# Kernel optimization log

Measured on AMD Instinct MI355X. Metric: run time of the kernel, lower is better.

Reference implementation:

```python
import jax, jax.numpy as jnp
import numpy as np

B, D, L, K = 4096, 1280, 16384, 64


def setup_inputs() -> dict:
    key = jax.random.key(0)
    k1, k2, k3, k4, k5 = jax.random.split(key, 5)
    scale_enc = 1.0 / np.sqrt(D)
    scale_dec = 1.0 / np.sqrt(L)
    return {
        "x_BD": jax.random.normal(k1, (B, D), dtype=jnp.float32),
        "pb_D": jax.random.normal(k2, (D,), dtype=jnp.float32) * 0.01,
        "W_enc": jax.random.normal(k3, (D, L), dtype=jnp.float32) * scale_enc,
        "lb_L": jax.random.normal(k4, (L,), dtype=jnp.float32) * 0.01,
        "W_dec": jax.random.normal(k5, (L, D), dtype=jnp.float32) * scale_dec,
    }


def topk_activation(x_BL, k):
    # lax.top_k over last dim, relu the values, scatter back into zeros
    tv_Bk, ti_Bk = jax.lax.top_k(x_BL, k)
    tv_Bk = jax.nn.relu(tv_Bk)
    b_B = jnp.arange(x_BL.shape[0])[:, None]
    return jnp.zeros_like(x_BL).at[b_B, ti_Bk].set(tv_Bk)


def reference(x_BD, pb_D, W_enc, lb_L, W_dec):
    # encode: shift by pre-bias, dense, add latent bias
    xshift_BD = x_BD - pb_D
    zpre_BL = xshift_BD @ W_enc + lb_L          # [B, L]
    # top-k sparse activation
    z_BL = topk_activation(zpre_BL, K)          # [B, L], only K nonzeros per row
    # decode: dense matmul over full L (the kernel-headroom target)
    xhat_BD = z_BL @ W_dec + pb_D               # [B, D]
    return (zpre_BL, z_BL, xhat_BD)
```

## Files before the change

### kernel.cpp

```cpp
#include <hip/hip_runtime.h>
#include <hip/hip_bf16.h>
#include <stdint.h>

#define B_SZ 4096
#define D_SZ 1280
#define L_SZ 16384
#define K_TOP 64
#define C_CAP 192
#define BAND 0.07f
#define CL_CAP 512
#define T_COLLECT 2.2f

typedef __attribute__((ext_vector_type(8))) short s16x8;
typedef __attribute__((ext_vector_type(4))) float f32x4;

#define GLOAD_LDS16(gp, lp)                                                          \
  __builtin_amdgcn_global_load_lds((const __attribute__((address_space(1))) void*)(gp), \
                                   (__attribute__((address_space(3))) void*)(lp), 16, 0, 0)

static __device__ __forceinline__ unsigned short f2bf(float f) {
  __hip_bfloat16 h = __float2bfloat16(f);
  return *reinterpret_cast<unsigned short*>(&h);
}
static __device__ __forceinline__ float bf2f(unsigned short u) {
  return __uint_as_float((unsigned)u << 16);
}
static __device__ __forceinline__ unsigned mkkey(float f) {
  const unsigned u = __float_as_uint(f);
  return (u & 0x80000000u) ? ~u : (u | 0x80000000u);
}
static __device__ __forceinline__ float unkey(unsigned k) {
  const unsigned u = (k & 0x80000000u) ? (k & 0x7fffffffu) : ~k;
  return __uint_as_float(u);
}
static __device__ __forceinline__ void nt_store4(const float4& v, float4* p) {
  f32x4 x;
  x[0] = v.x; x[1] = v.y; x[2] = v.z; x[3] = v.w;
  __builtin_nontemporal_store(x, (f32x4*)p);
}

__global__ __launch_bounds__(256) void sae_prep(const float* __restrict__ x,
                                                const float* __restrict__ pb,
                                                const float* __restrict__ We,
                                                const float* __restrict__ Wd,
                                                unsigned short* __restrict__ A,
                                                float* __restrict__ xs,
                                                float* __restrict__ WT,
                                                unsigned short* __restrict__ WbT,
                                                unsigned short* __restrict__ Wdb,
                                                int* __restrict__ bk_cnt,
                                                int* __restrict__ cl_cnt) {
  const int b = blockIdx.x, t = threadIdx.x;
  if (b < 5120) {
    __shared__ float tile[64][65];
    const int l0 = (b & 255) * 64, d0 = (b >> 8) * 64;
    const int c = t & 63, rg = t >> 6;
#pragma unroll
    for (int i = 0; i < 16; ++i) {
      const int row = i * 4 + rg;
      tile[row][c] = We[(size_t)(d0 + row) * L_SZ + l0 + c];
    }
    __syncthreads();
#pragma unroll
    for (int i = 0; i < 16; ++i) {
      const int row = i * 4 + rg;
      const float v = tile[c][row];
      const size_t o = (size_t)(l0 + row) * D_SZ + d0 + c;
      WT[o] = v;
      WbT[o] = f2bf(v);
    }
  } else if (b < 5120 + 4096) {
    const int r = b - 5120;
    const float* xr = x + (size_t)r * D_SZ;
    unsigned short* ar = A + (size_t)r * D_SZ;
    float* sr = xs + (size_t)r * D_SZ;
    for (int d = t; d < D_SZ; d += 256) {
      const float v = xr[d] - pb[d];
      ar[d] = f2bf(v);
      sr[d] = v;
    }
  } else if (b < 5120 + 4096 + 2048) {
    const int n4 = L_SZ * D_SZ / 4;
    for (int i = (b - 9216) * 256 + t; i < n4; i += 2048 * 256) {
      const float4 v = ((const float4*)Wd)[i];
      ushort4 o;
      o.x = f2bf(v.x); o.y = f2bf(v.y); o.z = f2bf(v.z); o.w = f2bf(v.w);
      ((ushort4*)Wdb)[i] = o;
    }
  } else if (b < 11328) {
    bk_cnt[(b - 11264) * 256 + t] = 0;
  } else {
    cl_cnt[(b - 11328) * 256 + t] = 0;
  }
}

#define SWZ(lin) ((lin) ^ ((((lin) >> 7) & 7) << 4))
#define A_LDS 0
#define B_LDS 65536
#define KBYTES (D_SZ * 2)

#define PH_MID()                                          \
  __builtin_amdgcn_s_barrier();                           \
  asm volatile("s_waitcnt lgkmcnt(0)" ::: "memory");      \
  __builtin_amdgcn_sched_barrier(0);                      \
  __builtin_amdgcn_s_setprio(1)

#define PH_END()                                          \
  __builtin_amdgcn_s_setprio(0);                          \
  __builtin_amdgcn_s_barrier();                           \
  __builtin_amdgcn_sched_barrier(0)

__global__ __launch_bounds__(512, 1) void sae_gemm(const unsigned short* __restrict__ A,
                                                   const unsigned short* __restrict__ WT,
                                                   const float* __restrict__ lb,
                                                   float* __restrict__ zpre,
                                                   int* __restrict__ cl_cnt,
                                                   int* __restrict__ cl_idx,
                                                   float* __restrict__ cl_val) {
  __shared__ short lds[65536];
  char* ldsc = (char*)lds;
  const int t = threadIdx.x, lane = t & 63, w = t >> 6;
  const int wr = w >> 2, wc = w & 3, w2 = w * 2;

  const int bid = blockIdx.x;
  const int xcd = bid & 7, i2 = bid >> 3;
  const int b2 = i2 >> 4, inner = i2 & 15;
  const int mt = (b2 & 3) * 4 + (inner & 3);
  const int nt = xcd * 8 + (b2 >> 2) * 4 + (inner >> 2);
  const int m0 = mt * 256, n0 = nt * 256;

  f32x4 acc[8][4] = {};

  auto STAGE = [&](const unsigned short* op, int rowbase, int ldsop, int buf, int half, int tile) {
#pragma unroll
    for (int s = 0; s < 2; ++s) {
      const int o = (w2 + s) * 1024 + lane * 16;
      const int r = o >> 7;
      const int cb = (o & 127) ^ (((o >> 7) & 7) << 4);
      const char* g = (const char*)op + (size_t)(rowbase + half * 128 + r) * KBYTES +
                      tile * 128 + cb;
      char* l = ldsc + ldsop + buf * 32768 + half * 16384 + (w2 + s) * 1024;
      GLOAD_LDS16(g, l);
    }
  };
  auto LDA = [&](s16x8* af, int buf, int q) {
#pragma unroll
    for (int i = 0; i < 2; ++i)
#pragma unroll
      for (int kk = 0; kk < 2; ++kk) {
        const int r = (q * 2 + i) * 16 + (lane & 15);
        int lin = r * 128 + kk * 64 + ((lane >> 4) * 16);
        lin = SWZ(lin);
        af[i * 2 + kk] = *(const s16x8*)(ldsc + A_LDS + buf * 32768 + wr * 16384 + lin);
      }
  };
  auto LDB = [&](s16x8* bg, int buf) {
#pragma unroll
    for (int j = 0; j < 4; ++j)
#pragma unroll
      for (int kk = 0; kk < 2; ++kk) {
        const int nloc = wc * 64 + j * 16 + (lane & 15);
        const int half = nloc >> 7, r = nloc & 127;
        int lin = r * 128 + kk * 64 + ((lane >> 4) * 16);
        lin = SWZ(lin);
        bg[j * 2 + kk] = *(const s16x8*)(ldsc + B_LDS + buf * 32768 + half * 16384 + lin);
      }
  };
  auto MM = [&](s16x8* af, s16x8* bg, int q) {
#pragma unroll
    for (int i = 0; i < 2; ++i)
#pragma unroll
      for (int j = 0; j < 4; ++j)
#pragma unroll
        for (int kk = 0; kk < 2; ++kk)
          acc[q * 2 + i][j] =
              __builtin_amdgcn_mfma_f32_16x16x32_bf16(af[i * 2 + kk], bg[j * 2 + kk],
                                                      acc[q * 2 + i][j], 0, 0, 0);
  };

  STAGE(WT, n0, B_LDS, 0, 0, 0); STAGE(WT, n0, B_LDS, 0, 1, 0);
  STAGE(A, m0, A_LDS, 0, 0, 0);  STAGE(A, m0, A_LDS, 0, 1, 0);
  STAGE(WT, n0, B_LDS, 1, 0, 1); STAGE(WT, n0, B_LDS, 1, 1, 1);
  asm volatile("s_waitcnt vmcnt(4)" ::: "memory");
  __builtin_amdgcn_s_barrier();
  __builtin_amdgcn_sched_barrier(0);

  const int NI = D_SZ / 128;
  for (int i = 0; i < NI; ++i) {
    const bool last = (i == NI - 1);
    s16x8 af[4], bg[8];
    LDB(bg, 0); LDA(af, 0, 0);
    STAGE(A, m0, A_LDS, 1, 0, 2 * i + 1); STAGE(A, m0, A_LDS, 1, 1, 2 * i + 1);
    PH_MID(); MM(af, bg, 0); PH_END();
    LDA(af, 0, 1);
    if (!last) STAGE(WT, n0, B_LDS, 0, 0, 2 * i + 2);
    PH_MID(); MM(af, bg, 1); PH_END();
    LDA(af, 0, 2);
    if (!last) STAGE(WT, n0, B_LDS, 0, 1, 2 * i + 2);
    PH_MID(); MM(af, bg, 2); PH_END();
    LDA(af, 0, 3);
    PH_MID(); MM(af, bg, 3);
    __builtin_amdgcn_s_setprio(0);
    if (last) { asm volatile("s_waitcnt vmcnt(0)" ::: "memory"); }
    else      { asm volatile("s_waitcnt vmcnt(4)" ::: "memory"); }
    __builtin_amdgcn_s_barrier();
    __builtin_amdgcn_sched_barrier(0);
    LDB(bg, 1); LDA(af, 1, 0);
    if (!last) STAGE(A, m0, A_LDS, 0, 0, 2 * i + 2);
    PH_MID(); MM(af, bg, 0); PH_END();
    LDA(af, 1, 1);
    if (!last) STAGE(A, m0, A_LDS, 0, 1, 2 * i + 2);
    PH_MID(); MM(af, bg, 1); PH_END();
    LDA(af, 1, 2);
    if (!last) STAGE(WT, n0, B_LDS, 1, 0, 2 * i + 3);
    PH_MID(); MM(af, bg, 2); PH_END();
    LDA(af, 1, 3);
    if (!last) STAGE(WT, n0, B_LDS, 1, 1, 2 * i + 3);
    PH_MID(); MM(af, bg, 3);
    __builtin_amdgcn_s_setprio(0);
    asm volatile("s_waitcnt vmcnt(4)" ::: "memory");
    __builtin_amdgcn_s_barrier();
    __builtin_amdgcn_sched_barrier(0);
  }

  const int cl = lane & 15, rg = lane >> 4;
#pragma unroll
  for (int j = 0; j < 4; ++j) {
    const int cc = n0 + wc * 64 + j * 16 + cl;
    const float bias = lb[cc];
#pragma unroll
    for (int i = 0; i < 8; ++i) {
      const int row0 = m0 + wr * 128 + i * 16 + rg * 4;
      const size_t base = (size_t)row0 * L_SZ + cc;
#pragma unroll
      for (int tt = 0; tt < 4; ++tt) {
        const float v = acc[i][j][tt] + bias;
        __builtin_nontemporal_store(v, &zpre[base + (size_t)tt * L_SZ]);
        if (v >= T_COLLECT) {
          const int p = atomicAdd(&cl_cnt[row0 + tt], 1);
          if (p < CL_CAP) {
            cl_idx[(size_t)(row0 + tt) * CL_CAP + p] = cc;
            cl_val[(size_t)(row0 + tt) * CL_CAP + p] = v;
          }
        }
      }
    }
  }
}

__device__ void radix_pick(unsigned* hist, unsigned* suf, int* sh_b, unsigned* sh_above,
                           int target, int t) {
  if (t == 0) *sh_b = -1;
  unsigned p = hist[4 * t] + hist[4 * t + 1] + hist[4 * t + 2] + hist[4 * t + 3];
  suf[t] = p;
  for (int off = 1; off < 256; off <<= 1) {
    __syncthreads();
    unsigned v = (t + off < 256) ? suf[t + off] : 0u;
    __syncthreads();
    suf[t] += v;
  }
  __syncthreads();
  const unsigned shi = (t + 1 < 256) ? suf[t + 1] : 0u;
  unsigned S = shi;
  int best = -1;
#pragma unroll
  for (int i = 3; i >= 0; --i) {
    S += hist[4 * t + i];
    if (S >= (unsigned)target) { best = 4 * t + i; break; }
  }
  if (best >= 0) atomicMax(sh_b, best);
  __syncthreads();
  const int b = *sh_b;
  if ((b >> 2) == t) {
    unsigned above = shi;
    for (int i = 3; i > (b & 3); --i) above += hist[4 * t + i];
    *sh_above = above;
  }
  __syncthreads();
}

__device__ void radix_pick4(unsigned* hist4, unsigned* suf, int* sh_b, unsigned* sh_above,
                            int target, int t) {
  if (t == 0) *sh_b = -1;
  if (t < 256) {
    unsigned p = 0;
#pragma unroll
    for (int i = 0; i < 4; ++i)
#pragma unroll
      for (int c = 0; c < 4; ++c) p += hist4[(4 * t + i) * 4 + c];
    suf[t] = p;
  }
  for (int off = 1; off < 256; off <<= 1) {
    __syncthreads();
    unsigned v = (t < 256 && t + off < 256) ? suf[t + off] : 0u;
    __syncthreads();
    if (t < 256) suf[t] += v;
  }
  __syncthreads();
  if (t < 256) {
    const unsigned shi = (t + 1 < 256) ? suf[t + 1] : 0u;
    unsigned S = shi;
    int best = -1;
    for (int i = 3; i >= 0; --i) {
      unsigned cnt = 0;
#pragma unroll
      for (int c = 0; c < 4; ++c) cnt += hist4[(4 * t + i) * 4 + c];
      S += cnt;
      if (S >= (unsigned)target) { best = 4 * t + i; break; }
    }
    if (best >= 0) atomicMax(sh_b, best);
  }
  __syncthreads();
  const int b = *sh_b;
  if (t < 256 && (b >> 2) == t) {
    unsigned above = (t + 1 < 256) ? suf[t + 1] : 0u;
    for (int i = 3; i > (b & 3); --i) {
      unsigned cnt = 0;
#pragma unroll
      for (int c = 0; c < 4; ++c) cnt += hist4[(4 * t + i) * 4 + c];
      above += cnt;
    }
    *sh_above = above;
  }
  __syncthreads();
}

__global__ __launch_bounds__(512) void sae_mega(const float* __restrict__ zpre,
                                                const float* __restrict__ xs,
                                                const float* __restrict__ WT,
                                                const float* __restrict__ lb,
                                                const unsigned short* __restrict__ Wdb,
                                                const float* __restrict__ pb,
                                                const int* __restrict__ cl_cnt,
                                                const int* __restrict__ cl_idx,
                                                const float* __restrict__ cl_val,
                                                float* __restrict__ z,
                                                float* __restrict__ xhat) {
  __shared__ unsigned hist4[4096];
  __shared__ unsigned suf[256];
  __shared__ int l_idx[CL_CAP];
  __shared__ unsigned l_key[CL_CAP];
  __shared__ int sh_b0, sh_b1, sh_nhi, sh_nband;
  __shared__ unsigned sh_above, sh_v64k;
  __shared__ int bl[C_CAP];
  __shared__ float bfv[C_CAP];
  __shared__ double be[C_CAP];
  __shared__ int ids[K_TOP];
  __shared__ float vs[K_TOP];

  const int r = blockIdx.x, t = threadIdx.x, lane = t & 63, w = t >> 6;
  const float4* zr4 = (const float4*)(zpre + (size_t)r * L_SZ);

  float4 xc[5];
  {
    const float4* xr4 = (const float4*)(xs + (size_t)r * D_SZ);
#pragma unroll
    for (int i = 0; i < 5; ++i) xc[i] = xr4[lane + 64 * i];
  }

  if (t == 0) { sh_nhi = 0; sh_nband = 0; }
  const int n_raw = cl_cnt[r];
  bool fast = (n_raw >= K_TOP && n_raw <= CL_CAP);
  float lo_f = 0.f, hi_f = 0.f;

  if (fast) {
    for (int i = t; i < n_raw; i += 512) {
      l_idx[i] = cl_idx[(size_t)r * CL_CAP + i];
      l_key[i] = mkkey(cl_val[(size_t)r * CL_CAP + i]);
    }
    __syncthreads();
    if (t < n_raw) {
      const unsigned myk = l_key[t];
      const int myi = l_idx[t];
      int rank = 0;
      for (int j = 0; j < n_raw; ++j) {
        const unsigned kj = l_key[j];
        rank += (kj > myk || (kj == myk && l_idx[j] < myi)) ? 1 : 0;
      }
      if (rank == K_TOP - 1) sh_v64k = myk;
    }
    __syncthreads();
    const float v64f = unkey(sh_v64k);
    lo_f = v64f - BAND;
    hi_f = v64f + BAND;
    if (T_COLLECT > lo_f) fast = false;
  }
  __syncthreads();
  if (!fast) {
    for (int i = t; i < 4096; i += 512) hist4[i] = 0;
    __syncthreads();
    for (int i = t; i < L_SZ / 4; i += 512) {
      const float4 v = zr4[i];
      const float va[4] = {v.x, v.y, v.z, v.w};
#pragma unroll
      for (int q = 0; q < 4; ++q)
        atomicAdd(&hist4[(mkkey(va[q]) >> 22) * 4 + (lane & 3)], 1u);
    }
    __syncthreads();
    radix_pick4(hist4, suf, &sh_b0, &sh_above, K_TOP, t);
    const int b0 = sh_b0;
    const int tgt2 = K_TOP - (int)sh_above;
    for (int i = t; i < 4096; i += 512) hist4[i] = 0;
    __syncthreads();
    for (int i = t; i < L_SZ / 4; i += 512) {
      const float4 v = zr4[i];
      const float va[4] = {v.x, v.y, v.z, v.w};
#pragma unroll
      for (int q = 0; q < 4; ++q) {
        const unsigned k = mkkey(va[q]);
        if ((int)(k >> 22) == b0) atomicAdd(&hist4[((k >> 12) & 1023u) * 4 + (lane & 3)], 1u);
      }
    }
    __syncthreads();
    radix_pick4(hist4, suf, &sh_b1, &sh_above, tgt2, t);
    const unsigned v64lb_key = (((unsigned)b0 << 10) | (unsigned)sh_b1) << 12;
    lo_f = unkey(v64lb_key) - BAND;
    hi_f = unkey(v64lb_key + 4095u) + BAND;
  }
  __syncthreads();
  if (fast) {
    if (t < n_raw) {
      const float val = unkey(l_key[t]);
      if (val >= lo_f) {
        if (val > hi_f) {
          const int p = atomicAdd(&sh_nhi, 1);
          if (p < K_TOP) { ids[p] = l_idx[t]; vs[p] = fmaxf(val, 0.f); }
        } else {
          const int p = atomicAdd(&sh_nband, 1);
          if (p < C_CAP) { bl[p] = l_idx[t]; bfv[p] = val; }
        }
      }
    }
  } else {
    for (int i = t; i < L_SZ / 4; i += 512) {
      const float4 v = zr4[i];
      const float va[4] = {v.x, v.y, v.z, v.w};
#pragma unroll
      for (int q = 0; q < 4; ++q) {
        const float val = va[q];
        if (val >= lo_f) {
          if (val > hi_f) {
            const int p = atomicAdd(&sh_nhi, 1);
            if (p < K_TOP) { ids[p] = 4 * i + q; vs[p] = fmaxf(val, 0.f); }
          } else {
            const int p = atomicAdd(&sh_nband, 1);
            if (p < C_CAP) { bl[p] = 4 * i + q; bfv[p] = val; }
          }
        }
      }
    }
  }
  __syncthreads();
  const int nh = sh_nhi < K_TOP ? sh_nhi : K_TOP;
  const int nb = sh_nband < C_CAP ? sh_nband : C_CAP;
  for (int e = w; e < nb; e += 8) {
    const int l = bl[e];
    const float4* wr4 = (const float4*)(WT + (size_t)l * D_SZ);
    double acc = 0.0;
#pragma unroll
    for (int i = 0; i < 5; ++i) {
      const float4 wv = wr4[lane + 64 * i];
      acc += (double)xc[i].x * (double)wv.x + (double)xc[i].y * (double)wv.y +
             (double)xc[i].z * (double)wv.z + (double)xc[i].w * (double)wv.w;
    }
#pragma unroll
    for (int off = 32; off > 0; off >>= 1) acc += __shfl_down(acc, off);
    if (lane == 0) be[e] = acc + (double)lb[l];
  }
  __syncthreads();
  const int need = K_TOP - nh;
  if (t < nb) {
    const double ev = be[t];
    const int l = bl[t];
    int rank = 0;
    for (int j = 0; j < nb; ++j) {
      const double e2 = be[j];
      if (e2 > ev || (e2 == ev && bl[j] < l)) ++rank;
    }
    if (rank < need) {
      ids[nh + rank] = l;
      vs[nh + rank] = fmaxf(bfv[t], 0.f);
    }
  }
  __syncthreads();
  if (t < 320) {
    float4 acc = ((const float4*)pb)[t];
#pragma unroll 8
    for (int k = 0; k < K_TOP; ++k) {
      const ushort4 wv = ((const ushort4*)(Wdb + (size_t)ids[k] * D_SZ))[t];
      const float vk = vs[k];
      acc.x += vk * bf2f(wv.x);
      acc.y += vk * bf2f(wv.y);
      acc.z += vk * bf2f(wv.z);
      acc.w += vk * bf2f(wv.w);
    }
    nt_store4(acc, &((float4*)(xhat + (size_t)r * D_SZ))[t]);
  } else {
    const int tz = t - 320;
    float4* zr = (float4*)(z + (size_t)r * L_SZ);
    const float4 zero = make_float4(0.f, 0.f, 0.f, 0.f);
    for (int i = tz; i < L_SZ / 4; i += 192) nt_store4(zero, &zr[i]);
  }
  __syncthreads();
  if (t < K_TOP) __builtin_nontemporal_store(vs[t], &z[(size_t)r * L_SZ + ids[t]]);
}

__global__ __launch_bounds__(256) void sae_topc(const float* __restrict__ zpre,
                                                int* __restrict__ bk_cnt,
                                                int* __restrict__ band_lat,
                                                float* __restrict__ band_fval,
                                                int* __restrict__ n_hi,
                                                int* __restrict__ n_band,
                                                int* __restrict__ t_idx,
                                                float* __restrict__ t_val) {
  __shared__ unsigned hist[1024];
  __shared__ unsigned suf[256];
  __shared__ int sh_b0, sh_b1, sh_nhi, sh_nband;
  __shared__ unsigned sh_above;
  const int r = blockIdx.x, t = threadIdx.x;
  const float4* zr4 = (const float4*)(zpre + (size_t)r * L_SZ);

  for (int i = t; i < 1024; i += 256) hist[i] = 0;
  if (t == 0) { sh_nhi = 0; sh_nband = 0; }
  __syncthreads();
  for (int i = t; i < L_SZ / 4; i += 256) {
    const float4 v = zr4[i];
    atomicAdd(&hist[mkkey(v.x) >> 22], 1u);
    atomicAdd(&hist[mkkey(v.y) >> 22], 1u);
    atomicAdd(&hist[mkkey(v.z) >> 22], 1u);
    atomicAdd(&hist[mkkey(v.w) >> 22], 1u);
  }
  __syncthreads();
  radix_pick(hist, suf, &sh_b0, &sh_above, K_TOP, t);
  const int b0 = sh_b0;
  const int target2 = K_TOP - (int)sh_above;
  __syncthreads();
  for (int i = t; i < 1024; i += 256) hist[i] = 0;
  __syncthreads();
  for (int i = t; i < L_SZ / 4; i += 256) {
    const float4 v = zr4[i];
    const float va[4] = {v.x, v.y, v.z, v.w};
#pragma unroll
    for (int q = 0; q < 4; ++q) {
      const unsigned k = mkkey(va[q]);
      if ((int)(k >> 22) == b0) atomicAdd(&hist[(k >> 12) & 1023u], 1u);
    }
  }
  __syncthreads();
  radix_pick(hist, suf, &sh_b1, &sh_above, target2, t);
  const unsigned v64lb_key = (((unsigned)b0 << 10) | (unsigned)sh_b1) << 12;
  const float lo_f = unkey(v64lb_key) - BAND;
  const float hi_f = unkey(v64lb_key + 4095u) + BAND;
  __syncthreads();
  for (int i = t; i < L_SZ / 4; i += 256) {
    const float4 v = zr4[i];
    const float va[4] = {v.x, v.y, v.z, v.w};
#pragma unroll
    for (int q = 0; q < 4; ++q) {
      const float val = va[q];
      if (val >= lo_f) {
        const int l = 4 * i + q;
        if (val > hi_f) {
          const int p = atomicAdd(&sh_nhi, 1);
          if (p < K_TOP) {
            t_idx[(size_t)r * K_TOP + p] = l;
            t_val[(size_t)r * K_TOP + p] = fmaxf(val, 0.f);
          }
        } else {
          const int p = atomicAdd(&sh_nband, 1);
          if (p < C_CAP) {
            band_lat[(r << 8) + p] = l;
            band_fval[(r << 8) + p] = val;
            atomicAdd(&bk_cnt[l], 1);
          }
        }
      }
    }
  }
  __syncthreads();
  if (t == 0) {
    n_hi[r] = sh_nhi < K_TOP ? sh_nhi : K_TOP;
    n_band[r] = sh_nband < C_CAP ? sh_nband : C_CAP;
  }
}

__global__ __launch_bounds__(256) void sae_scan(const int* __restrict__ counts,
                                                int* __restrict__ offsets,
                                                int* __restrict__ cursor) {
  __shared__ int part[256];
  const int t = threadIdx.x;
  int s = 0;
  for (int i = 0; i < 64; ++i) s += counts[t * 64 + i];
  part[t] = s;
  __syncthreads();
  int excl = 0;
  for (int j = 0; j < t; ++j) excl += part[j];
  int run = excl;
  for (int i = 0; i < 64; ++i) {
    const int idx = t * 64 + i;
    offsets[idx] = run;
    cursor[idx] = run;
    run += counts[idx];
  }
}

__global__ __launch_bounds__(192) void sae_bucket_fill(const int* __restrict__ band_lat,
                                                       const int* __restrict__ n_band,
                                                       int* __restrict__ cursor,
                                                       int* __restrict__ entries) {
  const int r = blockIdx.x, t = threadIdx.x;
  if (t < n_band[r]) {
    const int l = band_lat[(r << 8) + t];
    const int pos = atomicAdd(&cursor[l], 1);
    entries[pos] = (r << 8) | t;
  }
}

__global__ __launch_bounds__(256) void sae_refine_lm(const float* __restrict__ xs,
                                                     const float* __restrict__ WT,
                                                     const float* __restrict__ lb,
                                                     const int* __restrict__ counts,
                                                     const int* __restrict__ offsets,
                                                     const int* __restrict__ entries,
                                                     double* __restrict__ band_eval) {
  __shared__ float4 wl[D_SZ / 4];
  const int l = blockIdx.x;
  const int t = threadIdx.x, lane = t & 63, w = t >> 6;
  const int n = counts[l];
  if (n == 0) return;
  const float4* wc = (const float4*)(WT + (size_t)l * D_SZ);
  for (int d = t; d < D_SZ / 4; d += 256) wl[d] = wc[d];
  __syncthreads();
  const int base = offsets[l];
  const double bias = (double)lb[l];
  for (int e = w; e < n; e += 4) {
    const int ent = entries[base + e];
    const int rr = ent >> 8;
    const float4* xr = (const float4*)(xs + (size_t)rr * D_SZ);
    double acc = 0.0;
#pragma unroll
    for (int i = 0; i < 5; ++i) {
      const float4 xv = xr[lane + 64 * i];
      const float4 wv = wl[lane + 64 * i];
      acc += (double)xv.x * (double)wv.x + (double)xv.y * (double)wv.y +
             (double)xv.z * (double)wv.z + (double)xv.w * (double)wv.w;
    }
#pragma unroll
    for (int off = 32; off > 0; off >>= 1) acc += __shfl_down(acc, off);
    if (lane == 0) band_eval[ent] = acc + bias;
  }
}

__global__ __launch_bounds__(320) void sae_finish_nz(const int* __restrict__ n_hi,
                                                     const int* __restrict__ n_band,
                                                     const int* __restrict__ band_lat,
                                                     const float* __restrict__ band_fval,
                                                     const double* __restrict__ band_eval,
                                                     int* __restrict__ t_idx,
                                                     float* __restrict__ t_val,
                                                     const unsigned short* __restrict__ Wdb,
                                                     const float* __restrict__ pb,
                                                     float* __restrict__ xhat) {
  __shared__ int bl[C_CAP];
  __shared__ float bf[C_CAP];
  __shared__ double be[C_CAP];
  __shared__ int ids[K_TOP];
  __shared__ float vs[K_TOP];
  const int r = blockIdx.x, t = threadIdx.x;
  const int nh = n_hi[r], nb = n_band[r];
  if (t < nb) {
    bl[t] = band_lat[(r << 8) + t];
    bf[t] = band_fval[(r << 8) + t];
    be[t] = band_eval[(r << 8) + t];
  }
  if (t < nh) {
    ids[t] = t_idx[(size_t)r * K_TOP + t];
    vs[t] = t_val[(size_t)r * K_TOP + t];
  }
  __syncthreads();
  const int need = K_TOP - nh;
  if (t < nb) {
    const double ev = be[t];
    const int l = bl[t];
    int rank = 0;
    for (int j = 0; j < nb; ++j) {
      const double e2 = be[j];
      if (e2 > ev || (e2 == ev && bl[j] < l)) ++rank;
    }
    if (rank < need) {
      const float fv = fmaxf(bf[t], 0.f);
      ids[nh + rank] = l;
      vs[nh + rank] = fv;
      t_idx[(size_t)r * K_TOP + nh + rank] = l;
      t_val[(size_t)r * K_TOP + nh + rank] = fv;
    }
  }
  __syncthreads();
  float4 acc = ((const float4*)pb)[t];
#pragma unroll 8
  for (int k = 0; k < K_TOP; ++k) {
    const ushort4 wv = ((const ushort4*)(Wdb + (size_t)ids[k] * D_SZ))[t];
    const float vk = vs[k];
    acc.x += vk * bf2f(wv.x);
    acc.y += vk * bf2f(wv.y);
    acc.z += vk * bf2f(wv.z);
    acc.w += vk * bf2f(wv.w);
  }
  ((float4*)(xhat + (size_t)r * D_SZ))[t] = acc;
}

__global__ void sae_scatterA(const int* __restrict__ top_idx, const float* __restrict__ top_val,
                             float* __restrict__ z) {
  const int r = blockIdx.x;
  const int t = threadIdx.x;
  const int id = top_idx[(size_t)r * K_TOP + t];
  const float v = top_val[(size_t)r * K_TOP + t];
  z[(size_t)r * L_SZ + id] = v;
}

__global__ __launch_bounds__(256) void sae_scatterB(const int* __restrict__ top_idx,
                                                    const float* __restrict__ top_val,
                                                    float* __restrict__ z) {
  __shared__ int ids[32 * K_TOP];
  __shared__ float vs[32 * K_TOP];
  const int t = threadIdx.x;
  for (int i = t; i < 32 * K_TOP; i += 256) {
    ids[i] = top_idx[(size_t)4064 * K_TOP + i];
    vs[i] = top_val[(size_t)4064 * K_TOP + i];
  }
  __syncthreads();
  float4* zz = (float4*)(z + (size_t)4064 * L_SZ);
  for (int i = t; i < 32 * L_SZ / 4; i += 256) zz[i] = make_float4(0.f, 0.f, 0.f, 0.f);
  __syncthreads();
  for (int i = t; i < 32 * K_TOP; i += 256) {
    const int rr = 4064 + i / K_TOP;
    z[(size_t)rr * L_SZ + ids[i]] = vs[i];
  }
}

extern "C" void kernel_launch(void* const* d_in, const int* in_sizes, int n_in,
                              void* d_out, int out_size, void* d_ws, size_t ws_size,
                              hipStream_t stream) {
  const float* x  = (const float*)d_in[0];
  const float* pb = (const float*)d_in[1];
  const float* We = (const float*)d_in[2];
  const float* lb = (const float*)d_in[3];
  const float* Wd = (const float*)d_in[4];

  float* zpre = (float*)d_out;
  float* z    = zpre + (size_t)B_SZ * L_SZ;
  float* xhat = z + (size_t)B_SZ * L_SZ;

  const bool use_ws = ws_size >= ((size_t)251 << 20);
  char* sb = use_ws ? (char*)d_ws : (char*)z;

  unsigned short* A_bf   = (unsigned short*)(sb);
  unsigned short* WT_bf  = (unsigned short*)(sb + ((size_t)16 << 20));
  float*          WT_f32 = (float*)(sb + ((size_t)64 << 20));
  float*          xs_f32 = (float*)(sb + ((size_t)144 << 20));
  int*            b_lat  = (int*)(sb + ((size_t)164 << 20));
  float*          b_fval = (float*)(sb + ((size_t)168 << 20));
  double*         b_eval = (double*)(sb + ((size_t)172 << 20));
  int*            bk_cnt = (int*)(sb + ((size_t)180 << 20));
  int*            bk_off = (int*)(sb + ((size_t)181 << 20));
  int*            bk_cur = (int*)(sb + ((size_t)182 << 20));
  int*            bk_ent = (int*)(sb + ((size_t)184 << 20));
  unsigned short* Wd_bf  = (unsigned short*)(sb + ((size_t)188 << 20));
  int*            nhi_g  = (int*)(sb + ((size_t)228 << 20));
  int*            nbd_g  = (int*)(sb + ((size_t)229 << 20));
  int*            cl_idx = (int*)(sb + ((size_t)234 << 20));
  float*          cl_val = (float*)(sb + ((size_t)242 << 20));
  int*            cl_cnt = (int*)(sb + ((size_t)250 << 20));
  int*   t_idx = use_ws ? (int*)(sb + ((size_t)230 << 20))
                        : (int*)((char*)z + ((size_t)254 << 20));
  float* t_val = use_ws ? (float*)(sb + ((size_t)232 << 20))
                        : (float*)((char*)z + ((size_t)255 << 20));

  sae_prep<<<11344, 256, 0, stream>>>(x, pb, We, Wd, A_bf, xs_f32, WT_f32, WT_bf, Wd_bf,
                                      bk_cnt, cl_cnt);
  sae_gemm<<<1024, 512, 0, stream>>>(A_bf, WT_bf, lb, zpre, cl_cnt, cl_idx, cl_val);
  if (use_ws) {
    sae_mega<<<B_SZ, 512, 0, stream>>>(zpre, xs_f32, WT_f32, lb, Wd_bf, pb,
                                       cl_cnt, cl_idx, cl_val, z, xhat);
  } else {
    sae_topc<<<B_SZ, 256, 0, stream>>>(zpre, bk_cnt, b_lat, b_fval, nhi_g, nbd_g, t_idx, t_val);
    sae_scan<<<1, 256, 0, stream>>>(bk_cnt, bk_off, bk_cur);
    sae_bucket_fill<<<B_SZ, 192, 0, stream>>>(b_lat, nbd_g, bk_cur, bk_ent);
    sae_refine_lm<<<L_SZ, 256, 0, stream>>>(xs_f32, WT_f32, lb, bk_cnt, bk_off, bk_ent, b_eval);
    sae_finish_nz<<<B_SZ, 320, 0, stream>>>(nhi_g, nbd_g, b_lat, b_fval, b_eval, t_idx, t_val,
                                            Wd_bf, pb, xhat);
    hipMemsetAsync(z, 0, (size_t)4064 * L_SZ * sizeof(float), stream);
    sae_scatterA<<<4064, K_TOP, 0, stream>>>(t_idx, t_val, z);
    sae_scatterB<<<1, 256, 0, stream>>>(t_idx, t_val, z);
  }
}
```

Measured before the change: 662.3 us.

## Split fused mega kernel into select, decode, and z-write kernels

```diff
diff --git a/kernel.cpp b/kernel.cpp
--- a/kernel.cpp
+++ b/kernel.cpp
@@ -279,64 +279,16 @@
   __syncthreads();
 }
 
-__device__ void radix_pick4(unsigned* hist4, unsigned* suf, int* sh_b, unsigned* sh_above,
-                            int target, int t) {
-  if (t == 0) *sh_b = -1;
-  if (t < 256) {
-    unsigned p = 0;
-#pragma unroll
-    for (int i = 0; i < 4; ++i)
-#pragma unroll
-      for (int c = 0; c < 4; ++c) p += hist4[(4 * t + i) * 4 + c];
-    suf[t] = p;
-  }
-  for (int off = 1; off < 256; off <<= 1) {
-    __syncthreads();
-    unsigned v = (t < 256 && t + off < 256) ? suf[t + off] : 0u;
-    __syncthreads();
-    if (t < 256) suf[t] += v;
-  }
-  __syncthreads();
-  if (t < 256) {
-    const unsigned shi = (t + 1 < 256) ? suf[t + 1] : 0u;
-    unsigned S = shi;
-    int best = -1;
-    for (int i = 3; i >= 0; --i) {
-      unsigned cnt = 0;
-#pragma unroll
-      for (int c = 0; c < 4; ++c) cnt += hist4[(4 * t + i) * 4 + c];
-      S += cnt;
-      if (S >= (unsigned)target) { best = 4 * t + i; break; }
-    }
-    if (best >= 0) atomicMax(sh_b, best);
-  }
-  __syncthreads();
-  const int b = *sh_b;
-  if (t < 256 && (b >> 2) == t) {
-    unsigned above = (t + 1 < 256) ? suf[t + 1] : 0u;
-    for (int i = 3; i > (b & 3); --i) {
-      unsigned cnt = 0;
-#pragma unroll
-      for (int c = 0; c < 4; ++c) cnt += hist4[(4 * t + i) * 4 + c];
-      above += cnt;
-    }
-    *sh_above = above;
-  }
-  __syncthreads();
-}
-
-__global__ __launch_bounds__(512) void sae_mega(const float* __restrict__ zpre,
-                                                const float* __restrict__ xs,
-                                                const float* __restrict__ WT,
-                                                const float* __restrict__ lb,
-                                                const unsigned short* __restrict__ Wdb,
-                                                const float* __restrict__ pb,
-                                                const int* __restrict__ cl_cnt,
-                                                const int* __restrict__ cl_idx,
-                                                const float* __restrict__ cl_val,
-                                                float* __restrict__ z,
-                                                float* __restrict__ xhat) {
-  __shared__ unsigned hist4[4096];
+__global__ __launch_bounds__(256) void sae_select(const float* __restrict__ zpre,
+                                                  const float* __restrict__ xs,
+                                                  const float* __restrict__ WT,
+                                                  const float* __restrict__ lb,
+                                                  const int* __restrict__ cl_cnt,
+                                                  const int* __restrict__ cl_idx,
+                                                  const float* __restrict__ cl_val,
+                                                  int* __restrict__ t_idx,
+                                                  float* __restrict__ t_val) {
+  __shared__ unsigned hist[1024];
   __shared__ unsigned suf[256];
   __shared__ int l_idx[CL_CAP];
   __shared__ unsigned l_key[CL_CAP];
@@ -345,8 +297,6 @@
   __shared__ int bl[C_CAP];
   __shared__ float bfv[C_CAP];
   __shared__ double be[C_CAP];
-  __shared__ int ids[K_TOP];
-  __shared__ float vs[K_TOP];
 
   const int r = blockIdx.x, t = threadIdx.x, lane = t & 63, w = t >> 6;
   const float4* zr4 = (const float4*)(zpre + (size_t)r * L_SZ);
@@ -364,14 +314,14 @@
   float lo_f = 0.f, hi_f = 0.f;
 
   if (fast) {
-    for (int i = t; i < n_raw; i += 512) {
+    for (int i = t; i < n_raw; i += 256) {
       l_idx[i] = cl_idx[(size_t)r * CL_CAP + i];
       l_key[i] = mkkey(cl_val[(size_t)r * CL_CAP + i]);
     }
     __syncthreads();
-    if (t < n_raw) {
-      const unsigned myk = l_key[t];
-      const int myi = l_idx[t];
+    for (int it = t; it < n_raw; it += 256) {
+      const unsigned myk = l_key[it];
+      const int myi = l_idx[it];
       int rank = 0;
       for (int j = 0; j < n_raw; ++j) {
         const unsigned kj = l_key[j];
@@ -387,52 +337,56 @@
   }
   __syncthreads();
   if (!fast) {
-    for (int i = t; i < 4096; i += 512) hist4[i] = 0;
-    __syncthreads();
-    for (int i = t; i < L_SZ / 4; i += 512) {
+    for (int i = t; i < 1024; i += 256) hist[i] = 0;
+    __syncthreads();
+    for (int i = t; i < L_SZ / 4; i += 256) {
+      const float4 v = zr4[i];
+      atomicAdd(&hist[mkkey(v.x) >> 22], 1u);
+      atomicAdd(&hist[mkkey(v.y) >> 22], 1u);
+      atomicAdd(&hist[mkkey(v.z) >> 22], 1u);
+      atomicAdd(&hist[mkkey(v.w) >> 22], 1u);
+    }
+    __syncthreads();
+    radix_pick(hist, suf, &sh_b0, &sh_above, K_TOP, t);
+    const int b0 = sh_b0;
+    const int tgt2 = K_TOP - (int)sh_above;
+    __syncthreads();
+    for (int i = t; i < 1024; i += 256) hist[i] = 0;
+    __syncthreads();
+    for (int i = t; i < L_SZ / 4; i += 256) {
       const float4 v = zr4[i];
       const float va[4] = {v.x, v.y, v.z, v.w};
 #pragma unroll
-      for (int q = 0; q < 4; ++q)
-        atomicAdd(&hist4[(mkkey(va[q]) >> 22) * 4 + (lane & 3)], 1u);
-    }
-    __syncthreads();
-    radix_pick4(hist4, suf, &sh_b0, &sh_above, K_TOP, t);
-    const int b0 = sh_b0;
-    const int tgt2 = K_TOP - (int)sh_above;
-    for (int i = t; i < 4096; i += 512) hist4[i] = 0;
-    __syncthreads();
-    for (int i = t; i < L_SZ / 4; i += 512) {
-      const float4 v = zr4[i];
-      const float va[4] = {v.x, v.y, v.z, v.w};
-#pragma unroll
       for (int q = 0; q < 4; ++q) {
         const unsigned k = mkkey(va[q]);
-        if ((int)(k >> 22) == b0) atomicAdd(&hist4[((k >> 12) & 1023u) * 4 + (lane & 3)], 1u);
+        if ((int)(k >> 22) == b0) atomicAdd(&hist[(k >> 12) & 1023u], 1u);
       }
     }
     __syncthreads();
-    radix_pick4(hist4, suf, &sh_b1, &sh_above, tgt2, t);
+    radix_pick(hist, suf, &sh_b1, &sh_above, tgt2, t);
     const unsigned v64lb_key = (((unsigned)b0 << 10) | (unsigned)sh_b1) << 12;
     lo_f = unkey(v64lb_key) - BAND;
     hi_f = unkey(v64lb_key + 4095u) + BAND;
   }
   __syncthreads();
   if (fast) {
-    if (t < n_raw) {
-      const float val = unkey(l_key[t]);
+    for (int i = t; i < n_raw; i += 256) {
+      const float val = unkey(l_key[i]);
       if (val >= lo_f) {
         if (val > hi_f) {
           const int p = atomicAdd(&sh_nhi, 1);
-          if (p < K_TOP) { ids[p] = l_idx[t]; vs[p] = fmaxf(val, 0.f); }
+          if (p < K_TOP) {
+            t_idx[(size_t)r * K_TOP + p] = l_idx[i];
+            t_val[(size_t)r * K_TOP + p] = fmaxf(val, 0.f);
+          }
         } else {
           const int p = atomicAdd(&sh_nband, 1);
-          if (p < C_CAP) { bl[p] = l_idx[t]; bfv[p] = val; }
+          if (p < C_CAP) { bl[p] = l_idx[i]; bfv[p] = val; }
         }
       }
     }
   } else {
-    for (int i = t; i < L_SZ / 4; i += 512) {
+    for (int i = t; i < L_SZ / 4; i += 256) {
       const float4 v = zr4[i];
       const float va[4] = {v.x, v.y, v.z, v.w};
 #pragma unroll
@@ -441,7 +395,10 @@
         if (val >= lo_f) {
           if (val > hi_f) {
             const int p = atomicAdd(&sh_nhi, 1);
-            if (p < K_TOP) { ids[p] = 4 * i + q; vs[p] = fmaxf(val, 0.f); }
+            if (p < K_TOP) {
+              t_idx[(size_t)r * K_TOP + p] = 4 * i + q;
+              t_val[(size_t)r * K_TOP + p] = fmaxf(val, 0.f);
+            }
           } else {
             const int p = atomicAdd(&sh_nband, 1);
             if (p < C_CAP) { bl[p] = 4 * i + q; bfv[p] = val; }
@@ -453,7 +410,7 @@
   __syncthreads();
   const int nh = sh_nhi < K_TOP ? sh_nhi : K_TOP;
   const int nb = sh_nband < C_CAP ? sh_nband : C_CAP;
-  for (int e = w; e < nb; e += 8) {
+  for (int e = w; e < nb; e += 4) {
     const int l = bl[e];
     const float4* wr4 = (const float4*)(WT + (size_t)l * D_SZ);
     double acc = 0.0;
@@ -478,29 +435,53 @@
       if (e2 > ev || (e2 == ev && bl[j] < l)) ++rank;
     }
     if (rank < need) {
-      ids[nh + rank] = l;
-      vs[nh + rank] = fmaxf(bfv[t], 0.f);
-    }
-  }
-  __syncthreads();
-  if (t < 320) {
-    float4 acc = ((const float4*)pb)[t];
+      t_idx[(size_t)r * K_TOP + nh + rank] = l;
+      t_val[(size_t)r * K_TOP + nh + rank] = fmaxf(bfv[t], 0.f);
+    }
+  }
+}
+
+__global__ __launch_bounds__(320) void sae_decode2(const int* __restrict__ t_idx,
+                                                   const float* __restrict__ t_val,
+                                                   const unsigned short* __restrict__ Wdb,
+                                                   const float* __restrict__ pb,
+                                                   float* __restrict__ xhat) {
+  __shared__ int ids[K_TOP];
+  __shared__ float vs[K_TOP];
+  const int r = blockIdx.x, t = threadIdx.x;
+  if (t < K_TOP) {
+    ids[t] = t_idx[(size_t)r * K_TOP + t];
+    vs[t] = t_val[(size_t)r * K_TOP + t];
+  }
+  __syncthreads();
+  float4 acc = ((const float4*)pb)[t];
 #pragma unroll 8
-    for (int k = 0; k < K_TOP; ++k) {
-      const ushort4 wv = ((const ushort4*)(Wdb + (size_t)ids[k] * D_SZ))[t];
-      const float vk = vs[k];
-      acc.x += vk * bf2f(wv.x);
-      acc.y += vk * bf2f(wv.y);
-      acc.z += vk * bf2f(wv.z);
-      acc.w += vk * bf2f(wv.w);
-    }
-    nt_store4(acc, &((float4*)(xhat + (size_t)r * D_SZ))[t]);
-  } else {
-    const int tz = t - 320;
-    float4* zr = (float4*)(z + (size_t)r * L_SZ);
-    const float4 zero = make_float4(0.f, 0.f, 0.f, 0.f);
-    for (int i = tz; i < L_SZ / 4; i += 192) nt_store4(zero, &zr[i]);
-  }
+  for (int k = 0; k < K_TOP; ++k) {
+    const ushort4 wv = ((const ushort4*)(Wdb + (size_t)ids[k] * D_SZ))[t];
+    const float vk = vs[k];
+    acc.x += vk * bf2f(wv.x);
+    acc.y += vk * bf2f(wv.y);
+    acc.z += vk * bf2f(wv.z);
+    acc.w += vk * bf2f(wv.w);
+  }
+  nt_store4(acc, &((float4*)(xhat + (size_t)r * D_SZ))[t]);
+}
+
+__global__ __launch_bounds__(256) void sae_zwrite2(const int* __restrict__ t_idx,
+                                                   const float* __restrict__ t_val,
+                                                   float* __restrict__ z) {
+  __shared__ int ids[K_TOP];
+  __shared__ float vs[K_TOP];
+  const int r = blockIdx.x, t = threadIdx.x;
+  if (t < K_TOP) {
+    ids[t] = t_idx[(size_t)r * K_TOP + t];
+    vs[t] = t_val[(size_t)r * K_TOP + t];
+  }
+  __syncthreads();
+  float4* zr = (float4*)(z + (size_t)r * L_SZ);
+  const float4 zero = make_float4(0.f, 0.f, 0.f, 0.f);
+#pragma unroll
+  for (int i = 0; i < L_SZ / 4 / 256; ++i) nt_store4(zero, &zr[t + 256 * i]);
   __syncthreads();
   if (t < K_TOP) __builtin_nontemporal_store(vs[t], &z[(size_t)r * L_SZ + ids[t]]);
 }
@@ -780,8 +761,10 @@
                                       bk_cnt, cl_cnt);
   sae_gemm<<<1024, 512, 0, stream>>>(A_bf, WT_bf, lb, zpre, cl_cnt, cl_idx, cl_val);
   if (use_ws) {
-    sae_mega<<<B_SZ, 512, 0, stream>>>(zpre, xs_f32, WT_f32, lb, Wd_bf, pb,
-                                       cl_cnt, cl_idx, cl_val, z, xhat);
+    sae_select<<<B_SZ, 256, 0, stream>>>(zpre, xs_f32, WT_f32, lb, cl_cnt, cl_idx, cl_val,
+                                         t_idx, t_val);
+    sae_decode2<<<B_SZ, 320, 0, stream>>>(t_idx, t_val, Wd_bf, pb, xhat);
+    sae_zwrite2<<<B_SZ, 256, 0, stream>>>(t_idx, t_val, z);
   } else {
     sae_topc<<<B_SZ, 256, 0, stream>>>(zpre, bk_cnt, b_lat, b_fval, nhi_g, nbd_g, t_idx, t_val);
     sae_scan<<<1, 256, 0, stream>>>(bk_cnt, bk_off, bk_cur);
```

New measurement: 685.5 us. +3.5%, slower.
